# Kernel tuning notes

Hardware: AMD Instinct MI355X
Metric: run time of the kernel (lower is better)

The kernel has to match this reference:

```python
import jax, jax.numpy as jnp
import numpy as np
import math

B, T, L, M = 2, 16, 256, 512
D, H, DH, HT, ROT = 1024, 16, 64, 8, 32
EPS = 1e-5
NEG = jnp.float32(-1e9)
SCALE = 1.0 / math.sqrt(DH)


def _ln(x, g, b):
    mu = jnp.mean(x, -1, keepdims=True)
    var = jnp.mean((x - mu) ** 2, -1, keepdims=True)
    return (x - mu) * jax.lax.rsqrt(var + EPS) * g + b


def _rotate_half(x):
    x1, x2 = jnp.split(x, 2, axis=-1)
    return jnp.concatenate([-x2, x1], axis=-1)


def _apply_rope(t, pos):
    # t: (..., DH), pos broadcastable to (..., ROT)
    t_rot, t_pass = t[..., :ROT], t[..., ROT:]
    t_rot = t_rot * jnp.cos(pos) + _rotate_half(t_rot) * jnp.sin(pos)
    return jnp.concatenate([t_rot, t_pass], axis=-1)


def _decoder_layer(x, context, rope,
                   ca_ng, ca_nb, ca_cng, ca_cnb, ca_wq, ca_wkv, ca_wo,
                   ta_ng, ta_nb, ta_wqkv, ta_bqkv, ta_wo,
                   ff_ng, ff_nb, ff_w1, ff_w2,
                   context_mask, attn_mask):
    # ---- CrossAttention over flattened (t l) sequence ----
    xf = x.reshape(B, T * L, D)
    xn = _ln(xf, ca_ng, ca_nb)
    cn = _ln(context, ca_cng, ca_cnb)
    q = (xn @ ca_wq).reshape(B, T * L, H, DH)
    k, v = jnp.split(cn @ ca_wkv, 2, axis=-1)
    k = k.reshape(B, M, H, DH)
    v = v.reshape(B, M, H, DH)
    scores = jnp.einsum('bnhd,bmhd->bhnm', q, k) * SCALE
    scores = jnp.where(context_mask[:, None, None, :], scores, NEG)
    attn = jax.nn.softmax(scores, axis=-1)
    o = jnp.einsum('bhnm,bmhd->bnhd', attn, v).reshape(B, T * L, H * DH)
    x = x + (o @ ca_wo).reshape(B, T, L, D)

    # ---- PatchWiseTemporalAttention: attention over T at each spatial l ----
    xn = _ln(x, ta_ng, ta_nb)
    qkv = xn @ ta_wqkv + ta_bqkv  # (B,T,L,3*HT*DH)
    q, k, v = jnp.split(qkv, 3, axis=-1)
    q = q.reshape(B, T, L, HT, DH)
    k = k.reshape(B, T, L, HT, DH)
    v = v.reshape(B, T, L, HT, DH)
    # varlen rotary: masks are left-aligned so packed position == frame index t
    pos = rope[:, None, None, :]  # (T,1,1,ROT)
    q = _apply_rope(q, pos)
    k = _apply_rope(k, pos)
    scores = jnp.einsum('bqlhd,bklhd->blhqk', q, k) * SCALE
    scores = jnp.where(attn_mask[:, None, None, None, :], scores, NEG)
    attn = jax.nn.softmax(scores, axis=-1)
    o = jnp.einsum('blhqk,bklhd->bqlhd', attn, v).reshape(B, T, L, HT * DH)
    # pad_input fills zeros at invalid (masked) query rows before to_out (no bias)
    o = o * attn_mask[:, :, None, None].astype(o.dtype)
    x = x + o @ ta_wo

    # ---- FeedForward (LN -> Linear -> GELU(exact) -> Linear) ----
    h = jax.nn.gelu(_ln(x, ff_ng, ff_nb) @ ff_w1, approximate=False)
    x = x + h @ ff_w2
    return x


def setup_inputs():
    key = jax.random.key(0)
    ks = jax.random.split(key, 16)
    s = 0.02
    inner, inner_t, hid = H * DH, HT * DH, 4 * D
    lens = jax.random.randint(ks[0], (B,), 2, T + 1)
    attn_mask = jnp.arange(T)[None, :] < lens[:, None]  # left-aligned ragged lengths
    clens = jax.random.randint(ks[1], (B,), M // 2, M + 1)
    context_mask = jnp.arange(M)[None, :] < clens[:, None]
    return dict(
        x=jax.random.normal(ks[2], (B, T, L, D), jnp.float32),
        context=jax.random.normal(ks[3], (B, M, D), jnp.float32),
        rope=jax.random.normal(ks[4], (T, ROT), jnp.float32),
        ca_ng=jnp.ones((D,), jnp.float32), ca_nb=jnp.zeros((D,), jnp.float32),
        ca_cng=jnp.ones((D,), jnp.float32), ca_cnb=jnp.zeros((D,), jnp.float32),
        ca_wq=jax.random.normal(ks[5], (D, inner), jnp.float32) * s,
        ca_wkv=jax.random.normal(ks[6], (D, 2 * inner), jnp.float32) * s,
        ca_wo=jax.random.normal(ks[7], (inner, D), jnp.float32) * s,
        ta_ng=jnp.ones((D,), jnp.float32), ta_nb=jnp.zeros((D,), jnp.float32),
        ta_wqkv=jax.random.normal(ks[8], (D, 3 * inner_t), jnp.float32) * s,
        ta_bqkv=jnp.zeros((3 * inner_t,), jnp.float32),
        ta_wo=jax.random.normal(ks[9], (inner_t, D), jnp.float32) * s,
        ff_ng=jnp.ones((D,), jnp.float32), ff_nb=jnp.zeros((D,), jnp.float32),
        ff_w1=jax.random.normal(ks[10], (D, hid), jnp.float32) * s,
        ff_w2=jax.random.normal(ks[11], (hid, D), jnp.float32) * s,
        context_mask=context_mask,
        attn_mask=attn_mask,
    )


def reference(x, context, rope,
              ca_ng, ca_nb, ca_cng, ca_cnb, ca_wq, ca_wkv, ca_wo,
              ta_ng, ta_nb, ta_wqkv, ta_bqkv, ta_wo,
              ff_ng, ff_nb, ff_w1, ff_w2,
              context_mask, attn_mask):
    return _decoder_layer(x, context, rope,
                          ca_ng, ca_nb, ca_cng, ca_cnb, ca_wq, ca_wkv, ca_wo,
                          ta_ng, ta_nb, ta_wqkv, ta_bqkv, ta_wo,
                          ff_ng, ff_nb, ff_w1, ff_w2,
                          context_mask, attn_mask)
```

## Files before the change

### kernel.cpp

```cpp
#include <hip/hip_runtime.h>
#include <hip/hip_bf16.h>
#include <stdint.h>

#define DEV static __device__ __forceinline__

constexpr int kB = 2, kT = 16, kL = 256, kM = 512;
constexpr int kD = 1024, kH = 16, kDH = 64, kHT = 8, kROT = 32;
constexpr int kN = kT * kL;
constexpr float kEPS = 1e-5f;
constexpr float kNEG = -1.0e9f;
constexpr float kSCALE = 0.125f;

typedef __attribute__((ext_vector_type(8))) short short8;
typedef __attribute__((ext_vector_type(4))) float floatx4;
typedef __attribute__((ext_vector_type(16))) float floatx16;

DEV float b2f(__hip_bfloat16 v) { return __bfloat162float(v); }
DEV __hip_bfloat16 f2b(float v) { return __float2bfloat16(v); }
DEV float s2f(short x) {
  __hip_bfloat16_raw r; r.x = (unsigned short)x;
  return __bfloat162float(__hip_bfloat16(r));
}

DEV void gl2lds16(const __hip_bfloat16* g, __hip_bfloat16* l) {
  __builtin_amdgcn_global_load_lds(
      (const __attribute__((address_space(1))) void*)g,
      (__attribute__((address_space(3))) void*)l, 16, 0, 0);
}

struct TransArgs {
  const float* src[7];
  __hip_bfloat16* dst[7];
  const unsigned char* cmraw;
  const unsigned char* amraw;
  int* cmask;
  int* amask;
};
__constant__ const int kTKd[7] = {1024, 1024, 1024, 1024, 512, 1024, 4096};
__constant__ const int kTNd[7] = {1024, 2048, 1024, 1536, 1024, 4096, 1024};
__constant__ const int kTCum[8] = {0, 1024, 3072, 4096, 5632, 6144, 10240, 14336};

DEV int mask_val(const unsigned char* raw, int i) {
  unsigned char b1 = raw[1], b3 = raw[3];
  if (b1 == 0x3F) return ((const unsigned short*)raw)[i] != 0;
  if (b3 == 0x3F) return ((const float*)raw)[i] != 0.0f;
  if (b1 == 1)    return raw[i] != 0;
  return ((const int*)raw)[i] != 0;
}

__global__ __launch_bounds__(256) void transpose_all(TransArgs a) {
  int id = blockIdx.x;
  if (id >= 14336) {
    if (id == 14336) {
      for (int i = threadIdx.x; i < kB * kM; i += 256)
        a.cmask[i] = mask_val(a.cmraw, i);
    } else {
      if (threadIdx.x < kB * kT)
        a.amask[threadIdx.x] = mask_val(a.amraw, threadIdx.x);
    }
    return;
  }
  int seg = 0;
  #pragma unroll
  for (int s = 1; s < 7; s++) seg += (id >= kTCum[s]);
  unsigned t = id - kTCum[seg];
  int Kd = kTKd[seg], Nd = kTNd[seg];
  unsigned ntx = Nd / 32;
  int n0 = (t % ntx) * 32, k0 = (t / ntx) * 32;
  const float* W = a.src[seg];
  __hip_bfloat16* Wt = a.dst[seg];
  __shared__ float tile[32][33];
  int tx = threadIdx.x & 31, ty = threadIdx.x >> 5;
  for (int i = 0; i < 32; i += 8)
    tile[ty + i][tx] = W[(size_t)(k0 + ty + i) * Nd + n0 + tx];
  __syncthreads();
  for (int i = 0; i < 32; i += 8)
    Wt[(size_t)(n0 + ty + i) * Kd + k0 + tx] = f2b(tile[tx][ty + i]);
}

DEV void ln_body(const float* xr, const float* g, const float* bb,
                 __hip_bfloat16* outr, int tid) {
  float4 xv = *(const float4*)(xr + tid * 4);
  float s = xv.x + xv.y + xv.z + xv.w;
  float s2 = xv.x * xv.x + xv.y * xv.y + xv.z * xv.z + xv.w * xv.w;
  for (int off = 32; off; off >>= 1) {
    s += __shfl_down(s, off);
    s2 += __shfl_down(s2, off);
  }
  __shared__ float rs[4], rs2[4];
  if ((tid & 63) == 0) { rs[tid >> 6] = s; rs2[tid >> 6] = s2; }
  __syncthreads();
  float ts = rs[0] + rs[1] + rs[2] + rs[3];
  float ts2 = rs2[0] + rs2[1] + rs2[2] + rs2[3];
  float mu = ts * (1.f / kD);
  float var = ts2 * (1.f / kD) - mu * mu;
  float rstd = rsqrtf(var + kEPS);
  float4 gv = *(const float4*)(g + tid * 4);
  float4 bv = *(const float4*)(bb + tid * 4);
  ushort4 o;
  o.x = __hip_bfloat16_raw(f2b((xv.x - mu) * rstd * gv.x + bv.x)).x;
  o.y = __hip_bfloat16_raw(f2b((xv.y - mu) * rstd * gv.y + bv.y)).x;
  o.z = __hip_bfloat16_raw(f2b((xv.z - mu) * rstd * gv.z + bv.z)).x;
  o.w = __hip_bfloat16_raw(f2b((xv.w - mu) * rstd * gv.w + bv.w)).x;
  *(ushort4*)(outr + tid * 4) = o;
}

__global__ __launch_bounds__(256) void ln_rows(
    const float* __restrict__ X, const float* __restrict__ g,
    const float* __restrict__ bb, __hip_bfloat16* __restrict__ out) {
  int row = blockIdx.x;
  ln_body(X + (size_t)row * kD, g, bb, out + (size_t)row * kD, threadIdx.x);
}

__global__ __launch_bounds__(256) void ln_rows2(
    const float* __restrict__ X, const float* __restrict__ g,
    const float* __restrict__ bb, __hip_bfloat16* __restrict__ out,
    const float* __restrict__ X2, const float* __restrict__ g2,
    const float* __restrict__ bb2, __hip_bfloat16* __restrict__ out2) {
  int row = blockIdx.x;
  if (row < 8192)
    ln_body(X + (size_t)row * kD, g, bb, out + (size_t)row * kD, threadIdx.x);
  else {
    int r = row - 8192;
    ln_body(X2 + (size_t)r * kD, g2, bb2, out2 + (size_t)r * kD, threadIdx.x);
  }
}

DEV void gemm_epilogue(floatx16 acc[2][2], const float* bias, const float* res,
                       int gelu, void* out, int outBf16, int Nd,
                       int m0, int n0, int wm, int wn, int l32, int kg) {
  #pragma unroll
  for (int fa = 0; fa < 2; fa++) {
    #pragma unroll
    for (int fb = 0; fb < 2; fb++) {
      int col = n0 + wn + fb * 32 + l32;
      float bv = bias ? bias[col] : 0.f;
      #pragma unroll
      for (int r = 0; r < 16; r++) {
        int row = m0 + wm + fa * 32 + (r & 3) + 8 * (r >> 2) + 4 * kg;
        float v = acc[fa][fb][r] + bv;
        if (gelu) {
          v = v * (1.f / (1.f + __expf(-1.702f * v)));
        }
        size_t o = (size_t)row * Nd + col;
        if (res) v += res[o];
        if (outBf16) ((__hip_bfloat16*)out)[o] = f2b(v);
        else         ((float*)out)[o] = v;
      }
    }
  }
}

DEV void gemm_body(__hip_bfloat16* As, __hip_bfloat16* Bs,
                   const __hip_bfloat16* A, const __hip_bfloat16* Bt,
                   const float* bias, const float* res, int gelu,
                   void* out, int outBf16, int Nd, int Kd, int m0, int n0) {
  int tid = threadIdx.x, wave = tid >> 6, lane = tid & 63;
  int l32 = lane & 31, kg = lane >> 5;
  int wm = (wave >> 1) * 64, wn = (wave & 1) * 64;

  int srow = wave * 32 + (lane >> 3);
  int schunk8 = (((lane & 7) ^ ((lane >> 3) & 7)) << 3);
  const __hip_bfloat16* Ag = A + (size_t)(m0 + srow) * Kd + schunk8;
  const __hip_bfloat16* Bg = Bt + (size_t)(n0 + srow) * Kd + schunk8;
  __hip_bfloat16* Al = As + wave * 32 * 64;
  __hip_bfloat16* Bl = Bs + wave * 32 * 64;

  floatx16 acc[2][2] = {};
  for (int k0 = 0; k0 < Kd; k0 += 64) {
    #pragma unroll
    for (int i = 0; i < 4; i++) {
      gl2lds16(Ag + (size_t)(i * 8) * Kd + k0, Al + i * 512);
      gl2lds16(Bg + (size_t)(i * 8) * Kd + k0, Bl + i * 512);
    }
    __syncthreads();
    #pragma unroll
    for (int ks = 0; ks < 4; ks++) {
      int c = ks * 2 + kg;
      short8 af[2], bf2[2];
      #pragma unroll
      for (int fa = 0; fa < 2; fa++) {
        int row = wm + fa * 32 + l32;
        af[fa] = *(const short8*)(&As[row * 64 + (c ^ (row & 7)) * 8]);
      }
      #pragma unroll
      for (int fb = 0; fb < 2; fb++) {
        int row = wn + fb * 32 + l32;
        bf2[fb] = *(const short8*)(&Bs[row * 64 + (c ^ (row & 7)) * 8]);
      }
      #pragma unroll
      for (int fa = 0; fa < 2; fa++)
        #pragma unroll
        for (int fb = 0; fb < 2; fb++)
          acc[fa][fb] = __builtin_amdgcn_mfma_f32_32x32x16_bf16(
              af[fa], bf2[fb], acc[fa][fb], 0, 0, 0);
    }
    __syncthreads();
  }
  gemm_epilogue(acc, bias, res, gelu, out, outBf16, Nd, m0, n0, wm, wn, l32, kg);
}

__global__ __launch_bounds__(256) void gemm_bf16(
    const __hip_bfloat16* __restrict__ A, const __hip_bfloat16* __restrict__ Bt,
    const float* __restrict__ bias, const float* __restrict__ res, int gelu,
    void* __restrict__ out, int outBf16, int Nd, int Kd) {
  __shared__ __align__(16) __hip_bfloat16 As[128 * 64];
  __shared__ __align__(16) __hip_bfloat16 Bs[128 * 64];
  gemm_body(As, Bs, A, Bt, bias, res, gelu, out, outBf16, Nd, Kd,
            blockIdx.x * 128, blockIdx.y * 128);
}

__global__ __launch_bounds__(512, 2) void gemm_pipe(
    const __hip_bfloat16* __restrict__ A, const __hip_bfloat16* __restrict__ Bt,
    const float* __restrict__ bias, const float* __restrict__ res, int gelu,
    void* __restrict__ out, int outBf16, int Nd, int Kd) {
  __shared__ __align__(16) __hip_bfloat16 As[4][128 * 32];
  __shared__ __align__(16) __hip_bfloat16 Bs[4][256 * 32];
  const int m0 = blockIdx.x * 128, n0 = blockIdx.y * 256;
  const int tid = threadIdx.x, wave = tid >> 6, lane = tid & 63;
  const int l32 = lane & 31, kg = lane >> 5;
  const int wm = (wave >> 2) * 64, wn = (wave & 3) * 64;
  const int NT = Kd >> 5;

  const int arow = wave * 16 + (lane >> 2);
  const int alc = (lane & 3) ^ ((arow >> 1) & 3);
  const __hip_bfloat16* Ag = A + (size_t)(m0 + arow) * Kd + alc * 8;
  const int brow0 = wave * 32 + (lane >> 2);
  const int brow1 = brow0 + 16;
  const int blc0 = (lane & 3) ^ ((brow0 >> 1) & 3);
  const int blc1 = (lane & 3) ^ ((brow1 >> 1) & 3);
  const __hip_bfloat16* Bg0 = Bt + (size_t)(n0 + brow0) * Kd + blc0 * 8;
  const __hip_bfloat16* Bg1 = Bt + (size_t)(n0 + brow1) * Kd + blc1 * 8;
  __hip_bfloat16* Al = &As[0][0] + wave * 512;
  __hip_bfloat16* Bl0 = &Bs[0][0] + wave * 1024;
  __hip_bfloat16* Bl1 = Bl0 + 512;

  auto stage = [&](int t) {
    int slot = t & 3, k0 = t << 5;
    gl2lds16(Ag + k0, Al + slot * 4096);
    gl2lds16(Bg0 + k0, Bl0 + slot * 8192);
    gl2lds16(Bg1 + k0, Bl1 + slot * 8192);
  };

  floatx16 acc[2][2] = {};

  stage(0); stage(1); stage(2);
  asm volatile("s_waitcnt vmcnt(6)" ::: "memory");
  __builtin_amdgcn_s_barrier();
  asm volatile("" ::: "memory");

  for (int t = 0; t < NT; ++t) {
    const __hip_bfloat16* Asl = &As[t & 3][0];
    const __hip_bfloat16* Bsl = &Bs[t & 3][0];
    short8 af[2][2], bf2[2][2];
    #pragma unroll
    for (int ks = 0; ks < 2; ks++) {
      int c = ks * 2 + kg;
      #pragma unroll
      for (int fa = 0; fa < 2; fa++) {
        int row = wm + fa * 32 + l32;
        af[ks][fa] = *(const short8*)(Asl + row * 32 + (c ^ ((row >> 1) & 3)) * 8);
      }
      #pragma unroll
      for (int fb = 0; fb < 2; fb++) {
        int row = wn + fb * 32 + l32;
        bf2[ks][fb] = *(const short8*)(Bsl + row * 32 + (c ^ ((row >> 1) & 3)) * 8);
      }
    }
    if (t + 3 < NT) stage(t + 3);
    __builtin_amdgcn_s_barrier();
    asm volatile("s_waitcnt lgkmcnt(0)" ::: "memory");
    __builtin_amdgcn_s_setprio(1);
    #pragma unroll
    for (int ks = 0; ks < 2; ks++)
      #pragma unroll
      for (int fa = 0; fa < 2; fa++)
        #pragma unroll
        for (int fb = 0; fb < 2; fb++)
          acc[fa][fb] = __builtin_amdgcn_mfma_f32_32x32x16_bf16(
              af[ks][fa], bf2[ks][fb], acc[fa][fb], 0, 0, 0);
    __builtin_amdgcn_s_setprio(0);
    if (t < NT - 3)       asm volatile("s_waitcnt vmcnt(6)" ::: "memory");
    else if (t == NT - 3) asm volatile("s_waitcnt vmcnt(3)" ::: "memory");
    else if (t == NT - 2) asm volatile("s_waitcnt vmcnt(0)" ::: "memory");
    __builtin_amdgcn_s_barrier();
    asm volatile("" ::: "memory");
    __builtin_amdgcn_sched_barrier(0);
  }

  gemm_epilogue(acc, bias, res, gelu, out, outBf16, Nd, m0, n0, wm, wn, l32, kg);
}

__global__ __launch_bounds__(256) void cross_attn_mfma(
    const __hip_bfloat16* __restrict__ Qb,
    const __hip_bfloat16* __restrict__ KVb,
    const int* __restrict__ cmask,
    __hip_bfloat16* __restrict__ Ob) {
  __shared__ __align__(16) __hip_bfloat16 Vbf[2][8][64][8];
  __shared__ __align__(16) __hip_bfloat16 Paf[4][8][16][8];
  int b = blockIdx.y >> 4, h = blockIdx.y & 15;
  int q0 = blockIdx.x * 64;
  int tid = threadIdx.x, wave = tid >> 6, lane = tid & 63;
  int l16 = lane & 15, quad = lane >> 4;

  const __hip_bfloat16* qrow =
      Qb + (size_t)(b * kN + q0 + wave * 16 + l16) * 1024 + h * 64 + quad * 8;
  short8 qf0 = *(const short8*)qrow;
  short8 qf1 = *(const short8*)(qrow + 32);

  floatx4 of[4] = {};
  float Mr[4] = {-1e30f, -1e30f, -1e30f, -1e30f};
  float Lr[4] = {};

  int skey = tid >> 2, sd0 = (tid & 3) * 16;

  for (int kt = 0; kt < 8; kt++) {
    int buf = kt & 1;
    {
      const __hip_bfloat16* src =
          KVb + (size_t)(b * kM + kt * 64 + skey) * 2048 + 1024 + h * 64 + sd0;
      short8 v0 = *(const short8*)src;
      short8 v1 = *(const short8*)(src + 8);
      int kb = skey >> 3, kj = skey & 7;
      #pragma unroll
      for (int j = 0; j < 8; j++) {
        Vbf[buf][kb][sd0 + j][kj] = __hip_bfloat16(__hip_bfloat16_raw{(unsigned short)v0[j]});
        Vbf[buf][kb][sd0 + 8 + j][kj] = __hip_bfloat16(__hip_bfloat16_raw{(unsigned short)v1[j]});
      }
    }
    __syncthreads();

    floatx4 sf[4];
    #pragma unroll
    for (int nf = 0; nf < 4; nf++) {
      const __hip_bfloat16* krow =
          KVb + (size_t)(b * kM + kt * 64 + nf * 16 + l16) * 2048 + h * 64 + quad * 8;
      short8 kf0 = *(const short8*)krow;
      short8 kf1 = *(const short8*)(krow + 32);
      floatx4 z = {};
      z = __builtin_amdgcn_mfma_f32_16x16x32_bf16(qf0, kf0, z, 0, 0, 0);
      z = __builtin_amdgcn_mfma_f32_16x16x32_bf16(qf1, kf1, z, 0, 0, 0);
      sf[nf] = z;
    }

    float sv[4][4];
    #pragma unroll
    for (int nf = 0; nf < 4; nf++) {
      int mk = cmask[b * kM + kt * 64 + nf * 16 + l16];
      #pragma unroll
      for (int r = 0; r < 4; r++)
        sv[nf][r] = mk ? sf[nf][r] * kSCALE : kNEG;
    }
    float mx[4];
    #pragma unroll
    for (int r = 0; r < 4; r++) {
      float m = fmaxf(fmaxf(sv[0][r], sv[1][r]), fmaxf(sv[2][r], sv[3][r]));
      #pragma unroll
      for (int off = 1; off < 16; off <<= 1) m = fmaxf(m, __shfl_xor(m, off));
      mx[r] = m;
    }
    float alpha[4], Mn[4];
    #pragma unroll
    for (int r = 0; r < 4; r++) {
      Mn[r] = fmaxf(Mr[r], mx[r]);
      alpha[r] = __expf(Mr[r] - Mn[r]);
      Mr[r] = Mn[r];
    }
    float p[4][4];
    float rsum[4];
    #pragma unroll
    for (int r = 0; r < 4; r++) {
      float s = 0.f;
      #pragma unroll
      for (int nf = 0; nf < 4; nf++) {
        float e = __expf(sv[nf][r] - Mn[r]);
        p[nf][r] = e; s += e;
      }
      #pragma unroll
      for (int off = 1; off < 16; off <<= 1) s += __shfl_xor(s, off);
      rsum[r] = s;
    }
    #pragma unroll
    for (int r = 0; r < 4; r++) Lr[r] = Lr[r] * alpha[r] + rsum[r];
    #pragma unroll
    for (int df = 0; df < 4; df++)
      #pragma unroll
      for (int r = 0; r < 4; r++) of[df][r] *= alpha[r];

    #pragma unroll
    for (int nf = 0; nf < 4; nf++) {
      int col = nf * 16 + l16;
      int kb = col >> 3, kj = col & 7;
      #pragma unroll
      for (int r = 0; r < 4; r++)
        Paf[wave][kb][quad * 4 + r][kj] = f2b(p[nf][r]);
    }
    __builtin_amdgcn_s_waitcnt(0);

    short8 pf0 = *(const short8*)(&Paf[wave][quad][l16][0]);
    short8 pf1 = *(const short8*)(&Paf[wave][quad + 4][l16][0]);
    #pragma unroll
    for (int df = 0; df < 4; df++) {
      short8 vf0 = *(const short8*)(&Vbf[buf][quad][df * 16 + l16][0]);
      short8 vf1 = *(const short8*)(&Vbf[buf][quad + 4][df * 16 + l16][0]);
      of[df] = __builtin_amdgcn_mfma_f32_16x16x32_bf16(pf0, vf0, of[df], 0, 0, 0);
      of[df] = __builtin_amdgcn_mfma_f32_16x16x32_bf16(pf1, vf1, of[df], 0, 0, 0);
    }
  }

  #pragma unroll
  for (int df = 0; df < 4; df++) {
    #pragma unroll
    for (int r = 0; r < 4; r++) {
      int row = q0 + wave * 16 + quad * 4 + r;
      float v = of[df][r] / Lr[r];
      Ob[(size_t)(b * kN + row) * 1024 + h * 64 + df * 16 + l16] = f2b(v);
    }
  }
}

__global__ __launch_bounds__(64) void temporal_attn(
    const __hip_bfloat16* __restrict__ QKVb,
    const float* __restrict__ rope,
    const int* __restrict__ amask,
    __hip_bfloat16* __restrict__ Otb) {
  __shared__ float qs[16][65], ks[16][65], vs[16][65];
  __shared__ float Ps[16][17];
  int idx = blockIdx.x;
  int h = idx & 7, l = (idx >> 3) & 255, b = idx >> 11;
  int lane = threadIdx.x;

  {
    int tr = lane >> 2, c0 = (lane & 3) * 16;
    const __hip_bfloat16* base =
        QKVb + ((size_t)(b * kT + tr) * kL + l) * 1536 + h * 64;
    short8 qa = *(const short8*)(base + c0);
    short8 qb = *(const short8*)(base + c0 + 8);
    short8 ka = *(const short8*)(base + 512 + c0);
    short8 kb = *(const short8*)(base + 512 + c0 + 8);
    short8 va = *(const short8*)(base + 1024 + c0);
    short8 vb = *(const short8*)(base + 1024 + c0 + 8);
    #pragma unroll
    for (int j = 0; j < 8; j++) {
      qs[tr][c0 + j] = s2f(qa[j]) * kSCALE;
      qs[tr][c0 + 8 + j] = s2f(qb[j]) * kSCALE;
      ks[tr][c0 + j] = s2f(ka[j]);
      ks[tr][c0 + 8 + j] = s2f(kb[j]);
      vs[tr][c0 + j] = s2f(va[j]);
      vs[tr][c0 + 8 + j] = s2f(vb[j]);
    }
  }
  __syncthreads();
  {
    int rt = lane >> 2, rd0 = (lane & 3) * 8;
    float nq[8], nk[8];
    for (int j = 0; j < 8; j++) {
      int d = rd0 + j;
      float ang = rope[rt * kROT + d];
      float cv = cosf(ang), sv = sinf(ang);
      float oq = (d < 16) ? -qs[rt][d + 16] : qs[rt][d - 16];
      float ok = (d < 16) ? -ks[rt][d + 16] : ks[rt][d - 16];
      nq[j] = qs[rt][d] * cv + oq * sv;
      nk[j] = ks[rt][d] * cv + ok * sv;
    }
    __syncthreads();
    for (int j = 0; j < 8; j++) { qs[rt][rd0 + j] = nq[j]; ks[rt][rd0 + j] = nk[j]; }
  }
  __syncthreads();
  {
    int tq = lane >> 2, tk0 = (lane & 3) * 4;
    float s[4] = {0, 0, 0, 0};
    for (int d = 0; d < 64; d++) {
      float qv = qs[tq][d];
      s[0] += qv * ks[tk0 + 0][d];
      s[1] += qv * ks[tk0 + 1][d];
      s[2] += qv * ks[tk0 + 2][d];
      s[3] += qv * ks[tk0 + 3][d];
    }
    for (int jj = 0; jj < 4; jj++)
      Ps[tq][tk0 + jj] = amask[b * kT + tk0 + jj] ? s[jj] : kNEG;
  }
  __syncthreads();
  if (lane < 16) {
    float mx = -1e30f;
    for (int k = 0; k < 16; k++) mx = fmaxf(mx, Ps[lane][k]);
    float sum = 0.f;
    for (int k = 0; k < 16; k++) { float p = __expf(Ps[lane][k] - mx); Ps[lane][k] = p; sum += p; }
    float inv = 1.f / sum;
    for (int k = 0; k < 16; k++) Ps[lane][k] *= inv;
  }
  __syncthreads();
  for (int tq = 0; tq < 16; tq++) {
    float acc = 0.f;
    for (int tk = 0; tk < 16; tk++) acc += Ps[tq][tk] * vs[tk][lane];
    float qm = amask[b * kT + tq] ? 1.f : 0.f;
    Otb[((size_t)(b * kT + tq) * kL + l) * 512 + h * 64 + lane] = f2b(acc * qm);
  }
}

extern "C" void kernel_launch(void* const* d_in, const int* in_sizes, int n_in,
                              void* d_out, int out_size, void* d_ws, size_t ws_size,
                              hipStream_t stream) {
  const float* x       = (const float*)d_in[0];
  const float* ctx     = (const float*)d_in[1];
  const float* rope    = (const float*)d_in[2];
  const float* ca_ng   = (const float*)d_in[3];
  const float* ca_nb   = (const float*)d_in[4];
  const float* ca_cng  = (const float*)d_in[5];
  const float* ca_cnb  = (const float*)d_in[6];
  const float* ca_wq   = (const float*)d_in[7];
  const float* ca_wkv  = (const float*)d_in[8];
  const float* ca_wo   = (const float*)d_in[9];
  const float* ta_ng   = (const float*)d_in[10];
  const float* ta_nb   = (const float*)d_in[11];
  const float* ta_wqkv = (const float*)d_in[12];
  const float* ta_bqkv = (const float*)d_in[13];
  const float* ta_wo   = (const float*)d_in[14];
  const float* ff_ng   = (const float*)d_in[15];
  const float* ff_nb   = (const float*)d_in[16];
  const float* ff_w1   = (const float*)d_in[17];
  const float* ff_w2   = (const float*)d_in[18];
  const unsigned char* cmraw = (const unsigned char*)d_in[19];
  const unsigned char* amraw = (const unsigned char*)d_in[20];

  char* wsc = (char*)d_ws;
  size_t off = 0;
  auto take = [&](size_t bytes) {
    char* p = wsc + off;
    off = (off + bytes + 255) & ~(size_t)255;
    return p;
  };
  __hip_bfloat16* wqT   = (__hip_bfloat16*)take((size_t)1024 * 1024 * 2);
  __hip_bfloat16* wkvT  = (__hip_bfloat16*)take((size_t)2048 * 1024 * 2);
  __hip_bfloat16* woT   = (__hip_bfloat16*)take((size_t)1024 * 1024 * 2);
  __hip_bfloat16* wqkvT = (__hip_bfloat16*)take((size_t)1536 * 1024 * 2);
  __hip_bfloat16* tawoT = (__hip_bfloat16*)take((size_t)1024 * 512 * 2);
  __hip_bfloat16* ffw1T = (__hip_bfloat16*)take((size_t)4096 * 1024 * 2);
  __hip_bfloat16* ffw2T = (__hip_bfloat16*)take((size_t)1024 * 4096 * 2);
  __hip_bfloat16* XN  = (__hip_bfloat16*)take((size_t)8192 * 1024 * 2);
  __hip_bfloat16* CN  = (__hip_bfloat16*)take((size_t)1024 * 1024 * 2);
  __hip_bfloat16* Qb  = (__hip_bfloat16*)take((size_t)8192 * 1024 * 2);
  __hip_bfloat16* KVb = (__hip_bfloat16*)take((size_t)1024 * 2048 * 2);
  __hip_bfloat16* Ob  = (__hip_bfloat16*)take((size_t)8192 * 1024 * 2);
  float*          X1  = (float*)take((size_t)8192 * 1024 * 4);
  __hip_bfloat16* Hb  = (__hip_bfloat16*)take((size_t)8192 * 4096 * 2);
  int* cmask = (int*)take((size_t)kB * kM * 4);
  int* amask = (int*)take((size_t)kB * kT * 4);
  if (off > ws_size) return;

  __hip_bfloat16* QKVb = Hb;
  __hip_bfloat16* OTb  = Qb;

  auto gemmP = [&](const __hip_bfloat16* A, const __hip_bfloat16* Bt,
                   const float* bias, const float* res, int gelu, void* out,
                   int outBf16, int Md, int Nd, int Kd) {
    gemm_pipe<<<dim3(Md / 128, Nd / 256), dim3(512), 0, stream>>>(
        A, Bt, bias, res, gelu, out, outBf16, Nd, Kd);
  };

  TransArgs ta;
  ta.src[0] = ca_wq;   ta.dst[0] = wqT;
  ta.src[1] = ca_wkv;  ta.dst[1] = wkvT;
  ta.src[2] = ca_wo;   ta.dst[2] = woT;
  ta.src[3] = ta_wqkv; ta.dst[3] = wqkvT;
  ta.src[4] = ta_wo;   ta.dst[4] = tawoT;
  ta.src[5] = ff_w1;   ta.dst[5] = ffw1T;
  ta.src[6] = ff_w2;   ta.dst[6] = ffw2T;
  ta.cmraw = cmraw; ta.amraw = amraw; ta.cmask = cmask; ta.amask = amask;
  transpose_all<<<dim3(14338), dim3(256), 0, stream>>>(ta);

  ln_rows2<<<dim3(9216), dim3(256), 0, stream>>>(x, ca_ng, ca_nb, XN,
                                                 ctx, ca_cng, ca_cnb, CN);
  gemmP(XN, wqT, nullptr, nullptr, 0, Qb, 1, 8192, 1024, 1024);
  gemm_bf16<<<dim3(8, 16), dim3(256), 0, stream>>>(
      CN, wkvT, nullptr, nullptr, 0, KVb, 1, 2048, 1024);
  cross_attn_mfma<<<dim3(kN / 64, kB * kH), dim3(256), 0, stream>>>(Qb, KVb, cmask, Ob);
  gemmP(Ob, woT, nullptr, x, 0, X1, 0, 8192, 1024, 1024);

  ln_rows<<<dim3(8192), dim3(256), 0, stream>>>(X1, ta_ng, ta_nb, XN);
  gemmP(XN, wqkvT, ta_bqkv, nullptr, 0, QKVb, 1, 8192, 1536, 1024);
  temporal_attn<<<dim3(kB * kL * kHT), dim3(64), 0, stream>>>(QKVb, rope, amask, OTb);
  gemmP(OTb, tawoT, nullptr, X1, 0, X1, 0, 8192, 1024, 512);

  ln_rows<<<dim3(8192), dim3(256), 0, stream>>>(X1, ff_ng, ff_nb, XN);
  gemmP(XN, ffw1T, nullptr, nullptr, 1, Hb, 1, 8192, 4096, 1024);
  gemmP(Hb, ffw2T, nullptr, X1, 0, d_out, 0, 8192, 1024, 4096);
}
```

Before: 683.1 us.

## Replace pipelined GEMM with 256x256 ping-pong kernel and fuse Q/KV projections

```diff
diff --git a/kernel.cpp b/kernel.cpp
--- a/kernel.cpp
+++ b/kernel.cpp
@@ -126,9 +126,52 @@
   }
 }
 
-DEV void gemm_epilogue(floatx16 acc[2][2], const float* bias, const float* res,
-                       int gelu, void* out, int outBf16, int Nd,
-                       int m0, int n0, int wm, int wn, int l32, int kg) {
+DEV void gemm_body(__hip_bfloat16* As, __hip_bfloat16* Bs,
+                   const __hip_bfloat16* A, const __hip_bfloat16* Bt,
+                   const float* bias, const float* res, int gelu,
+                   void* out, int outBf16, int Nd, int Kd, int m0, int n0) {
+  int tid = threadIdx.x, wave = tid >> 6, lane = tid & 63;
+  int l32 = lane & 31, kg = lane >> 5;
+  int wm = (wave >> 1) * 64, wn = (wave & 1) * 64;
+
+  int srow = wave * 32 + (lane >> 3);
+  int schunk8 = (((lane & 7) ^ ((lane >> 3) & 7)) << 3);
+  const __hip_bfloat16* Ag = A + (size_t)(m0 + srow) * Kd + schunk8;
+  const __hip_bfloat16* Bg = Bt + (size_t)(n0 + srow) * Kd + schunk8;
+  __hip_bfloat16* Al = As + wave * 32 * 64;
+  __hip_bfloat16* Bl = Bs + wave * 32 * 64;
+
+  floatx16 acc[2][2] = {};
+  for (int k0 = 0; k0 < Kd; k0 += 64) {
+    #pragma unroll
+    for (int i = 0; i < 4; i++) {
+      gl2lds16(Ag + (size_t)(i * 8) * Kd + k0, Al + i * 512);
+      gl2lds16(Bg + (size_t)(i * 8) * Kd + k0, Bl + i * 512);
+    }
+    __syncthreads();
+    #pragma unroll
+    for (int ks = 0; ks < 4; ks++) {
+      int c = ks * 2 + kg;
+      short8 af[2], bf2[2];
+      #pragma unroll
+      for (int fa = 0; fa < 2; fa++) {
+        int row = wm + fa * 32 + l32;
+        af[fa] = *(const short8*)(&As[row * 64 + (c ^ (row & 7)) * 8]);
+      }
+      #pragma unroll
+      for (int fb = 0; fb < 2; fb++) {
+        int row = wn + fb * 32 + l32;
+        bf2[fb] = *(const short8*)(&Bs[row * 64 + (c ^ (row & 7)) * 8]);
+      }
+      #pragma unroll
+      for (int fa = 0; fa < 2; fa++)
+        #pragma unroll
+        for (int fb = 0; fb < 2; fb++)
+          acc[fa][fb] = __builtin_amdgcn_mfma_f32_32x32x16_bf16(
+              af[fa], bf2[fb], acc[fa][fb], 0, 0, 0);
+    }
+    __syncthreads();
+  }
   #pragma unroll
   for (int fa = 0; fa < 2; fa++) {
     #pragma unroll
@@ -151,55 +194,6 @@
   }
 }
 
-DEV void gemm_body(__hip_bfloat16* As, __hip_bfloat16* Bs,
-                   const __hip_bfloat16* A, const __hip_bfloat16* Bt,
-                   const float* bias, const float* res, int gelu,
-                   void* out, int outBf16, int Nd, int Kd, int m0, int n0) {
-  int tid = threadIdx.x, wave = tid >> 6, lane = tid & 63;
-  int l32 = lane & 31, kg = lane >> 5;
-  int wm = (wave >> 1) * 64, wn = (wave & 1) * 64;
-
-  int srow = wave * 32 + (lane >> 3);
-  int schunk8 = (((lane & 7) ^ ((lane >> 3) & 7)) << 3);
-  const __hip_bfloat16* Ag = A + (size_t)(m0 + srow) * Kd + schunk8;
-  const __hip_bfloat16* Bg = Bt + (size_t)(n0 + srow) * Kd + schunk8;
-  __hip_bfloat16* Al = As + wave * 32 * 64;
-  __hip_bfloat16* Bl = Bs + wave * 32 * 64;
-
-  floatx16 acc[2][2] = {};
-  for (int k0 = 0; k0 < Kd; k0 += 64) {
-    #pragma unroll
-    for (int i = 0; i < 4; i++) {
-      gl2lds16(Ag + (size_t)(i * 8) * Kd + k0, Al + i * 512);
-      gl2lds16(Bg + (size_t)(i * 8) * Kd + k0, Bl + i * 512);
-    }
-    __syncthreads();
-    #pragma unroll
-    for (int ks = 0; ks < 4; ks++) {
-      int c = ks * 2 + kg;
-      short8 af[2], bf2[2];
-      #pragma unroll
-      for (int fa = 0; fa < 2; fa++) {
-        int row = wm + fa * 32 + l32;
-        af[fa] = *(const short8*)(&As[row * 64 + (c ^ (row & 7)) * 8]);
-      }
-      #pragma unroll
-      for (int fb = 0; fb < 2; fb++) {
-        int row = wn + fb * 32 + l32;
-        bf2[fb] = *(const short8*)(&Bs[row * 64 + (c ^ (row & 7)) * 8]);
-      }
-      #pragma unroll
-      for (int fa = 0; fa < 2; fa++)
-        #pragma unroll
-        for (int fb = 0; fb < 2; fb++)
-          acc[fa][fb] = __builtin_amdgcn_mfma_f32_32x32x16_bf16(
-              af[fa], bf2[fb], acc[fa][fb], 0, 0, 0);
-    }
-    __syncthreads();
-  }
-  gemm_epilogue(acc, bias, res, gelu, out, outBf16, Nd, m0, n0, wm, wn, l32, kg);
-}
-
 __global__ __launch_bounds__(256) void gemm_bf16(
     const __hip_bfloat16* __restrict__ A, const __hip_bfloat16* __restrict__ Bt,
     const float* __restrict__ bias, const float* __restrict__ res, int gelu,
@@ -210,85 +204,181 @@
             blockIdx.x * 128, blockIdx.y * 128);
 }
 
-__global__ __launch_bounds__(512, 2) void gemm_pipe(
+__global__ __launch_bounds__(256) void gemm_pair(
+    const __hip_bfloat16* __restrict__ A0, const __hip_bfloat16* __restrict__ B0,
+    void* __restrict__ o0,
+    const __hip_bfloat16* __restrict__ A1, const __hip_bfloat16* __restrict__ B1,
+    void* __restrict__ o1) {
+  __shared__ __align__(16) __hip_bfloat16 As[128 * 64];
+  __shared__ __align__(16) __hip_bfloat16 Bs[128 * 64];
+  int id = blockIdx.x;
+  if (id < 512) {
+    gemm_body(As, Bs, A0, B0, nullptr, nullptr, 0, o0, 1, 1024, 1024,
+              (id & 63) * 128, (id >> 6) * 128);
+  } else {
+    int r = id - 512;
+    gemm_body(As, Bs, A1, B1, nullptr, nullptr, 0, o1, 1, 2048, 1024,
+              (r & 7) * 128, (r >> 3) * 128);
+  }
+}
+
+__global__ __launch_bounds__(512, 2) void gemm_8p(
     const __hip_bfloat16* __restrict__ A, const __hip_bfloat16* __restrict__ Bt,
     const float* __restrict__ bias, const float* __restrict__ res, int gelu,
     void* __restrict__ out, int outBf16, int Nd, int Kd) {
-  __shared__ __align__(16) __hip_bfloat16 As[4][128 * 32];
-  __shared__ __align__(16) __hip_bfloat16 Bs[4][256 * 32];
-  const int m0 = blockIdx.x * 128, n0 = blockIdx.y * 256;
+  __shared__ __align__(16) __hip_bfloat16 As[2][256][64];
+  __shared__ __align__(16) __hip_bfloat16 Bs[2][256][64];
+  const int m0 = blockIdx.x * 256, n0 = blockIdx.y * 256;
   const int tid = threadIdx.x, wave = tid >> 6, lane = tid & 63;
   const int l32 = lane & 31, kg = lane >> 5;
-  const int wm = (wave >> 2) * 64, wn = (wave & 3) * 64;
-  const int NT = Kd >> 5;
-
-  const int arow = wave * 16 + (lane >> 2);
-  const int alc = (lane & 3) ^ ((arow >> 1) & 3);
-  const __hip_bfloat16* Ag = A + (size_t)(m0 + arow) * Kd + alc * 8;
-  const int brow0 = wave * 32 + (lane >> 2);
-  const int brow1 = brow0 + 16;
-  const int blc0 = (lane & 3) ^ ((brow0 >> 1) & 3);
-  const int blc1 = (lane & 3) ^ ((brow1 >> 1) & 3);
-  const __hip_bfloat16* Bg0 = Bt + (size_t)(n0 + brow0) * Kd + blc0 * 8;
-  const __hip_bfloat16* Bg1 = Bt + (size_t)(n0 + brow1) * Kd + blc1 * 8;
-  __hip_bfloat16* Al = &As[0][0] + wave * 512;
-  __hip_bfloat16* Bl0 = &Bs[0][0] + wave * 1024;
-  __hip_bfloat16* Bl1 = Bl0 + 512;
-
-  auto stage = [&](int t) {
-    int slot = t & 3, k0 = t << 5;
-    gl2lds16(Ag + k0, Al + slot * 4096);
-    gl2lds16(Bg0 + k0, Bl0 + slot * 8192);
-    gl2lds16(Bg1 + k0, Bl1 + slot * 8192);
-  };
-
-  floatx16 acc[2][2] = {};
-
-  stage(0); stage(1); stage(2);
+  const int wm = (wave >> 2) * 128;
+  const int wn = (wave & 3) * 64;
+  const int NT = Kd >> 6;
+  const int NI = NT >> 1;
+
+  const int srow = (wave << 3) + (lane >> 3);
+  const int swz8 = (((lane & 7) ^ ((lane >> 3) & 7)) << 3);
+  const __hip_bfloat16* Agt = A + (size_t)(m0 + srow) * Kd + swz8;
+  const __hip_bfloat16* Bgt = Bt + (size_t)(n0 + srow) * Kd + swz8;
+
+  auto stA = [&](int buf, int hf, int t) {
+    const __hip_bfloat16* g = Agt + (size_t)(hf * 128) * Kd + t * 64;
+    __hip_bfloat16* l = &As[buf][hf * 128 + (wave << 3)][0];
+    gl2lds16(g, l);
+    gl2lds16(g + (size_t)64 * Kd, l + 64 * 64);
+  };
+  auto stB = [&](int buf, int hf, int t) {
+    const __hip_bfloat16* g = Bgt + (size_t)(hf * 128) * Kd + t * 64;
+    __hip_bfloat16* l = &Bs[buf][hf * 128 + (wave << 3)][0];
+    gl2lds16(g, l);
+    gl2lds16(g + (size_t)64 * Kd, l + 64 * 64);
+  };
+  auto ldA4 = [&](int buf, int mf, short8* d) {
+    int row = wm + mf * 32 + l32;
+    const __hip_bfloat16* p = &As[buf][row][0];
+    #pragma unroll
+    for (int ks = 0; ks < 4; ks++) {
+      int c = ks * 2 + kg;
+      d[ks] = *(const short8*)(p + ((c ^ (row & 7)) << 3));
+    }
+  };
+  auto ldB8 = [&](int buf, short8* d) {
+    #pragma unroll
+    for (int fb = 0; fb < 2; fb++) {
+      int row = wn + fb * 32 + l32;
+      const __hip_bfloat16* p = &Bs[buf][row][0];
+      #pragma unroll
+      for (int ks = 0; ks < 4; ks++) {
+        int c = ks * 2 + kg;
+        d[fb * 4 + ks] = *(const short8*)(p + ((c ^ (row & 7)) << 3));
+      }
+    }
+  };
+
+  floatx16 acc[4][2] = {};
+  auto phase_mid = [&] {
+    asm volatile("" ::: "memory");
+    __builtin_amdgcn_s_barrier();
+    asm volatile("s_waitcnt lgkmcnt(0)" ::: "memory");
+    __builtin_amdgcn_sched_barrier(0);
+  };
+  auto phase_end = [&] {
+    asm volatile("" ::: "memory");
+    __builtin_amdgcn_s_barrier();
+    asm volatile("" ::: "memory");
+  };
+
+  short8 aA[4], aB[4], b[8];
+
+  #define MMAQ(mf, ar)                                                      \
+    __builtin_amdgcn_s_setprio(1);                                          \
+    _Pragma("unroll")                                                       \
+    for (int ks = 0; ks < 4; ks++) {                                        \
+      acc[mf][0] = __builtin_amdgcn_mfma_f32_32x32x16_bf16(                 \
+          ar[ks], b[ks], acc[mf][0], 0, 0, 0);                              \
+      acc[mf][1] = __builtin_amdgcn_mfma_f32_32x32x16_bf16(                 \
+          ar[ks], b[4 + ks], acc[mf][1], 0, 0, 0);                          \
+    }                                                                       \
+    __builtin_amdgcn_s_setprio(0);
+
+  stB(0, 0, 0); stB(0, 1, 0); stA(0, 0, 0); stA(0, 1, 0);
+  stB(1, 0, 1); stB(1, 1, 1); stA(1, 0, 1);
   asm volatile("s_waitcnt vmcnt(6)" ::: "memory");
   __builtin_amdgcn_s_barrier();
   asm volatile("" ::: "memory");
-
-  for (int t = 0; t < NT; ++t) {
-    const __hip_bfloat16* Asl = &As[t & 3][0];
-    const __hip_bfloat16* Bsl = &Bs[t & 3][0];
-    short8 af[2][2], bf2[2][2];
-    #pragma unroll
-    for (int ks = 0; ks < 2; ks++) {
-      int c = ks * 2 + kg;
-      #pragma unroll
-      for (int fa = 0; fa < 2; fa++) {
-        int row = wm + fa * 32 + l32;
-        af[ks][fa] = *(const short8*)(Asl + row * 32 + (c ^ ((row >> 1) & 3)) * 8);
+  ldA4(0, 0, aA);
+
+  for (int i = 0; i < NI; ++i) {
+    const int ta = 2 * i, tb = ta + 1;
+    const bool more = (i + 1 < NI);
+    ldB8(0, b);
+    ldA4(0, 1, aB);
+    stA(1, 1, tb);
+    phase_mid();
+    MMAQ(0, aA);
+    phase_end();
+    ldA4(0, 2, aA);
+    if (more) stB(0, 0, ta + 2);
+    phase_mid();
+    MMAQ(1, aB);
+    phase_end();
+    ldA4(0, 3, aB);
+    if (more) stB(0, 1, ta + 2);
+    phase_mid();
+    MMAQ(2, aA);
+    if (more) asm volatile("s_waitcnt vmcnt(4)" ::: "memory");
+    else      asm volatile("s_waitcnt vmcnt(0)" ::: "memory");
+    phase_end();
+    ldA4(1, 0, aA);
+    if (more) stA(0, 0, ta + 2);
+    phase_mid();
+    MMAQ(3, aB);
+    phase_end();
+    ldB8(1, b);
+    ldA4(1, 1, aB);
+    if (more) stA(0, 1, ta + 2);
+    phase_mid();
+    MMAQ(0, aA);
+    phase_end();
+    ldA4(1, 2, aA);
+    if (more) stB(1, 0, tb + 2);
+    phase_mid();
+    MMAQ(1, aB);
+    phase_end();
+    ldA4(1, 3, aB);
+    if (more) stB(1, 1, tb + 2);
+    phase_mid();
+    MMAQ(2, aA);
+    if (more) asm volatile("s_waitcnt vmcnt(4)" ::: "memory");
+    phase_end();
+    if (more) {
+      ldA4(0, 0, aA);
+      stA(1, 0, tb + 2);
+    }
+    phase_mid();
+    MMAQ(3, aB);
+    phase_end();
+  }
+  #undef MMAQ
+
+  #pragma unroll
+  for (int mf = 0; mf < 4; mf++) {
+    #pragma unroll
+    for (int fb = 0; fb < 2; fb++) {
+      int col = n0 + wn + fb * 32 + l32;
+      float bv = bias ? bias[col] : 0.f;
+      #pragma unroll
+      for (int r = 0; r < 16; r++) {
+        int row = m0 + wm + mf * 32 + (r & 3) + 8 * (r >> 2) + 4 * kg;
+        float v = acc[mf][fb][r] + bv;
+        if (gelu) v = v * (1.f / (1.f + __expf(-1.702f * v)));
+        size_t o = (size_t)row * Nd + col;
+        if (res) v += res[o];
+        if (outBf16) ((__hip_bfloat16*)out)[o] = f2b(v);
+        else         ((float*)out)[o] = v;
       }
-      #pragma unroll
-      for (int fb = 0; fb < 2; fb++) {
-        int row = wn + fb * 32 + l32;
-        bf2[ks][fb] = *(const short8*)(Bsl + row * 32 + (c ^ ((row >> 1) & 3)) * 8);
-      }
-    }
-    if (t + 3 < NT) stage(t + 3);
-    __builtin_amdgcn_s_barrier();
-    asm volatile("s_waitcnt lgkmcnt(0)" ::: "memory");
-    __builtin_amdgcn_s_setprio(1);
-    #pragma unroll
-    for (int ks = 0; ks < 2; ks++)
-      #pragma unroll
-      for (int fa = 0; fa < 2; fa++)
-        #pragma unroll
-        for (int fb = 0; fb < 2; fb++)
-          acc[fa][fb] = __builtin_amdgcn_mfma_f32_32x32x16_bf16(
-              af[ks][fa], bf2[ks][fb], acc[fa][fb], 0, 0, 0);
-    __builtin_amdgcn_s_setprio(0);
-    if (t < NT - 3)       asm volatile("s_waitcnt vmcnt(6)" ::: "memory");
-    else if (t == NT - 3) asm volatile("s_waitcnt vmcnt(3)" ::: "memory");
-    else if (t == NT - 2) asm volatile("s_waitcnt vmcnt(0)" ::: "memory");
-    __builtin_amdgcn_s_barrier();
-    asm volatile("" ::: "memory");
-    __builtin_amdgcn_sched_barrier(0);
-  }
-
-  gemm_epilogue(acc, bias, res, gelu, out, outBf16, Nd, m0, n0, wm, wn, l32, kg);
+    }
+  }
 }
 
 __global__ __launch_bounds__(256) void cross_attn_mfma(
@@ -551,10 +641,16 @@
   __hip_bfloat16* QKVb = Hb;
   __hip_bfloat16* OTb  = Qb;
 
-  auto gemmP = [&](const __hip_bfloat16* A, const __hip_bfloat16* Bt,
+  auto gemm = [&](const __hip_bfloat16* A, const __hip_bfloat16* Bt,
+                  const float* bias, const float* res, int gelu, void* out,
+                  int outBf16, int Md, int Nd, int Kd) {
+    gemm_bf16<<<dim3(Md / 128, Nd / 128), dim3(256), 0, stream>>>(
+        A, Bt, bias, res, gelu, out, outBf16, Nd, Kd);
+  };
+  auto gemm8 = [&](const __hip_bfloat16* A, const __hip_bfloat16* Bt,
                    const float* bias, const float* res, int gelu, void* out,
                    int outBf16, int Md, int Nd, int Kd) {
-    gemm_pipe<<<dim3(Md / 128, Nd / 256), dim3(512), 0, stream>>>(
+    gemm_8p<<<dim3(Md / 256, Nd / 256), dim3(512), 0, stream>>>(
         A, Bt, bias, res, gelu, out, outBf16, Nd, Kd);
   };
 
@@ -571,18 +667,16 @@
 
   ln_rows2<<<dim3(9216), dim3(256), 0, stream>>>(x, ca_ng, ca_nb, XN,
                                                  ctx, ca_cng, ca_cnb, CN);
-  gemmP(XN, wqT, nullptr, nullptr, 0, Qb, 1, 8192, 1024, 1024);
-  gemm_bf16<<<dim3(8, 16), dim3(256), 0, stream>>>(
-      CN, wkvT, nullptr, nullptr, 0, KVb, 1, 2048, 1024);
+  gemm_pair<<<dim3(640), dim3(256), 0, stream>>>(XN, wqT, Qb, CN, wkvT, KVb);
   cross_attn_mfma<<<dim3(kN / 64, kB * kH), dim3(256), 0, stream>>>(Qb, KVb, cmask, Ob);
-  gemmP(Ob, woT, nullptr, x, 0, X1, 0, 8192, 1024, 1024);
+  gemm(Ob, woT, nullptr, x, 0, X1, 0, 8192, 1024, 1024);
 
   ln_rows<<<dim3(8192), dim3(256), 0, stream>>>(X1, ta_ng, ta_nb, XN);
-  gemmP(XN, wqkvT, ta_bqkv, nullptr, 0, QKVb, 1, 8192, 1536, 1024);
+  gemm8(XN, wqkvT, ta_bqkv, nullptr, 0, QKVb, 1, 8192, 1536, 1024);
   temporal_attn<<<dim3(kB * kL * kHT), dim3(64), 0, stream>>>(QKVb, rope, amask, OTb);
-  gemmP(OTb, tawoT, nullptr, X1, 0, X1, 0, 8192, 1024, 512);
+  gemm(OTb, tawoT, nullptr, X1, 0, X1, 0, 8192, 1024, 512);
 
   ln_rows<<<dim3(8192), dim3(256), 0, stream>>>(X1, ff_ng, ff_nb, XN);
-  gemmP(XN, ffw1T, nullptr, nullptr, 1, Hb, 1, 8192, 4096, 1024);
-  gemmP(Hb, ffw2T, nullptr, X1, 0, d_out, 0, 8192, 1024, 4096);
-}
+  gemm8(XN, ffw1T, nullptr, nullptr, 1, Hb, 1, 8192, 4096, 1024);
+  gemm(Hb, ffw2T, nullptr, X1, 0, d_out, 0, 8192, 1024, 4096);
+}
```

Measured after the change: 651.2 us. 1.05x faster.
